# Kernel tuning notes

Measured on AMD Instinct MI355X. Metric: run time of the kernel, lower is better.

## Reference

```python
import jax, jax.numpy as jnp
import numpy as np

B, S, D, H = 4, 1024, 1024, 16
HD = D // H  # head_dim = 64


def setup_inputs() -> dict:
    key = jax.random.key(0)
    ks = jax.random.split(key, 18)
    s = 0.02
    return {
        "x": jax.random.normal(ks[0], (B, S, D), jnp.float32),
        "trust_scores": jax.random.uniform(ks[1], (B, S), jnp.float32),
        "mask": jax.random.randint(ks[2], (B, S), 0, 2).astype(jnp.int32),
        # Linear weights stored as (in, out); torch does x @ W.T + b, equivalent here.
        "Wq": jax.random.normal(ks[3], (D, D), jnp.float32) * s,
        "bq": jnp.zeros((D,), jnp.float32),
        "Wk": jax.random.normal(ks[4], (D, D), jnp.float32) * s,
        "bk": jnp.zeros((D,), jnp.float32),
        "Wv": jax.random.normal(ks[5], (D, D), jnp.float32) * s,
        "bv": jnp.zeros((D,), jnp.float32),
        "Wtp": jax.random.normal(ks[6], (1, HD), jnp.float32) * s,
        "btp": jnp.zeros((HD,), jnp.float32),
        "Wg": jax.random.normal(ks[7], (D + 1, D), jnp.float32) * s,
        "bg": jnp.zeros((D,), jnp.float32),
        "Wo": jax.random.normal(ks[8], (D, D), jnp.float32) * s,
        "bo": jnp.zeros((D,), jnp.float32),
    }


def reference(x, trust_scores, mask, Wq, bq, Wk, bk, Wv, bv, Wtp, btp, Wg, bg, Wo, bo):
    b, s, d = x.shape
    hd = Wtp.shape[1]
    h = d // hd
    # QKV projections -> [b, h, s, hd]
    q = (x @ Wq + bq).reshape(b, s, h, hd).transpose(0, 2, 1, 3)
    k = (x @ Wk + bk).reshape(b, s, h, hd).transpose(0, 2, 1, 3)
    v = (x @ Wv + bv).reshape(b, s, h, hd).transpose(0, 2, 1, 3)
    scores = jnp.einsum("bhqd,bhkd->bhqk", q, k) / jnp.sqrt(jnp.float32(hd))
    # Trust affinity bias: project scalar trust -> head_dim, outer-product + sigmoid.
    trust_proj = trust_scores[:, :, None] @ Wtp + btp  # [b, s, hd]
    trust_aff = jax.nn.sigmoid(jnp.einsum("bqd,bkd->bqk", trust_proj, trust_proj))
    scores = scores + 0.1 * trust_aff[:, None, :, :]  # broadcast over heads
    # Mask applies along the QUERY axis (mask.unsqueeze(1).unsqueeze(-1) in torch).
    scores = jnp.where(mask[:, None, :, None] == 0, jnp.float32(-1e9), scores)
    attn = jax.nn.softmax(scores, axis=-1)  # [b, h, s, s]
    attended = jnp.einsum("bhqk,bhkd->bhqd", attn, v)
    attended = attended.transpose(0, 2, 1, 3).reshape(b, s, d)
    # Trust gate: sigmoid(Linear([attended, trust])) elementwise gate.
    gate_in = jnp.concatenate([attended, trust_scores[:, :, None]], axis=-1)
    gate = jax.nn.sigmoid(gate_in @ Wg + bg)
    attended = attended * gate
    output = attended @ Wo + bo
    return (output, attn)
```

## Files before the change

kernel.cpp:

```cpp
#include <hip/hip_runtime.h>
#include <math.h>

#define BB 4
#define SS 1024
#define DD 1024
#define HH 16
#define HDD 64
#define MTOT (BB*SS)
#define MB (1024*1024)

typedef float  f32x4  __attribute__((ext_vector_type(4)));
typedef __bf16 bf16x8 __attribute__((ext_vector_type(8)));
typedef unsigned short u16;

__device__ __forceinline__ unsigned short f2bf(float f) {
    union { float f; unsigned u; } v; v.f = f;
    unsigned r = v.u + 0x7FFFu + ((v.u >> 16) & 1u);
    return (unsigned short)(r >> 16);
}
__device__ __forceinline__ float bf2f(unsigned short u) {
    union { unsigned u; float f; } v; v.u = ((unsigned)u) << 16;
    return v.f;
}
__device__ __forceinline__ f32x4 mfma16(bf16x8 a, bf16x8 b, f32x4 c) {
    return __builtin_amdgcn_mfma_f32_16x16x32_bf16(a, b, c, 0, 0, 0);
}
__device__ __forceinline__ void gload16(const void* g, void* l) {
    __builtin_amdgcn_global_load_lds(
        (const __attribute__((address_space(1))) void*)g,
        (__attribute__((address_space(3))) void*)l, 16, 0, 0);
}
__device__ __forceinline__ void lds_fence() {
    asm volatile("s_waitcnt lgkmcnt(0)" ::: "memory");
    __builtin_amdgcn_sched_barrier(0);
}

__global__ void split_kernel(const float* __restrict__ in, u16* __restrict__ hi,
                             u16* __restrict__ lo, int n4)
{
    for (int i = blockIdx.x*blockDim.x + threadIdx.x; i < n4; i += gridDim.x*blockDim.x) {
        f32x4 v = ((const f32x4*)in)[i];
        ushort4 h4;
        h4.x = f2bf(v[0]); h4.y = f2bf(v[1]); h4.z = f2bf(v[2]); h4.w = f2bf(v[3]);
        ((ushort4*)hi)[i] = h4;
        if (lo) {
            ushort4 l4v;
            l4v.x = f2bf(v[0] - bf2f(h4.x)); l4v.y = f2bf(v[1] - bf2f(h4.y));
            l4v.z = f2bf(v[2] - bf2f(h4.z)); l4v.w = f2bf(v[3] - bf2f(h4.w));
            ((ushort4*)lo)[i] = l4v;
        }
    }
}

__global__ __launch_bounds__(256)
void tsplit5_kernel(const float* W0, u16* h0,
                    const float* W1, u16* h1,
                    const float* W2, u16* h2,
                    const float* W3, u16* h3,
                    const float* W4, u16* h4, u16* l4T)
{
    const float* W; u16* hT; u16* lT = nullptr;
    switch (blockIdx.z) {
        case 0: W = W0; hT = h0; break;
        case 1: W = W1; hT = h1; break;
        case 2: W = W2; hT = h2; break;
        case 3: W = W3; hT = h3; break;
        default: W = W4; hT = h4; lT = l4T; break;
    }
    __shared__ float tile[64][65];
    const int t  = threadIdx.x;
    const int k0 = blockIdx.y * 64, n0 = blockIdx.x * 64;
    const int r  = t >> 4, c4 = (t & 15) * 4;
    #pragma unroll
    for (int rr = 0; rr < 4; ++rr) {
        const int k = r + rr*16;
        f32x4 v = *(const f32x4*)&W[(size_t)(k0 + k)*1024 + n0 + c4];
        tile[k][c4+0] = v[0]; tile[k][c4+1] = v[1]; tile[k][c4+2] = v[2]; tile[k][c4+3] = v[3];
    }
    __syncthreads();
    #pragma unroll
    for (int rr = 0; rr < 4; ++rr) {
        const int nl = r + rr*16;
        ushort4 hh, ll;
        {
            float v;
            v = tile[c4+0][nl]; hh.x = f2bf(v); ll.x = f2bf(v - bf2f(hh.x));
            v = tile[c4+1][nl]; hh.y = f2bf(v); ll.y = f2bf(v - bf2f(hh.y));
            v = tile[c4+2][nl]; hh.z = f2bf(v); ll.z = f2bf(v - bf2f(hh.z));
            v = tile[c4+3][nl]; hh.w = f2bf(v); ll.w = f2bf(v - bf2f(hh.w));
        }
        *(ushort4*)&hT[(size_t)(n0 + nl)*1024 + k0 + c4] = hh;
        if (lT) *(ushort4*)&lT[(size_t)(n0 + nl)*1024 + k0 + c4] = ll;
    }
}

__global__ void tconst_kernel(const float* __restrict__ Wtp, const float* __restrict__ btp,
                              float* __restrict__ out3)
{
    const int l = threadIdx.x;
    const float w = Wtp[l], b = btp[l];
    float a = w*w, m = w*b, c = b*b;
    #pragma unroll
    for (int s = 32; s; s >>= 1) {
        a += __shfl_down(a, s);
        m += __shfl_down(m, s);
        c += __shfl_down(c, s);
    }
    if (l == 0) { out3[0] = a; out3[1] = m; out3[2] = c; }
}

__global__ __launch_bounds__(256)
void tbias_kernel(const float* __restrict__ trust, const float* __restrict__ tconst,
                  u16* __restrict__ T2)
{
    const int qt = blockIdx.x;
    const int b  = blockIdx.y;
    const int t  = threadIdx.x;
    const int lane = t & 63, grp = t >> 6;
    const int l15 = lane & 15, l4 = lane >> 4;
    const float c1 = tconst[0], c2 = tconst[1], c3 = tconst[2];
    float tq[4];
    #pragma unroll
    for (int r = 0; r < 4; ++r) tq[r] = trust[b*SS + qt*16 + l4*4 + r];
    for (int kt2 = 0; kt2 < 16; ++kt2) {
        const int kt = grp*16 + kt2;
        const float tk = trust[b*SS + kt*16 + l15];
        ushort4 o;
        #pragma unroll
        for (int r = 0; r < 4; ++r) {
            const float ta = c1*tq[r]*tk + c2*(tq[r] + tk) + c3;
            ((u16*)&o)[r] = f2bf(0.1f/(1.f + __expf(-ta)));
        }
        *(ushort4*)&T2[((((size_t)b*64 + qt)*64 + kt)*64 + lane)*4] = o;
    }
}

template<int MODE, int PASSES>
__global__ __launch_bounds__(256)
void mgemm(const u16* __restrict__ Ah, const u16* __restrict__ Al,
           const u16* __restrict__ Bh, const u16* __restrict__ Bl,
           const float* __restrict__ bias,
           float* __restrict__ outF, u16* __restrict__ outH, u16* __restrict__ outL,
           int M, int N,
           const float* __restrict__ trust, const float* __restrict__ wlast,
           const u16* __restrict__ attH, const u16* __restrict__ attL)
{
    constexpr int NT   = (PASSES == 3) ? 4 : (PASSES == 2) ? 3 : 2;
    constexpr int BIDX = (PASSES == 1) ? 1 : 2;
    __shared__ u16 lds[2][NT][128*64];

    const int t    = threadIdx.x;
    const int lane = t & 63, wave = t >> 6;
    const int l15  = lane & 15, l4 = lane >> 4;
    const int wr   = wave >> 1, wc = wave & 1;
    const int w64  = wave << 6;
    const int m0   = blockIdx.y * 128, n0 = blockIdx.x * 128;

    const u16* srcs[NT];
    srcs[0] = Ah + (size_t)m0*1024;
    if (PASSES >= 2) srcs[1] = Al + (size_t)m0*1024;
    if (MODE == 6) {
        srcs[BIDX] = (n0 < 1024) ? Bh + (size_t)n0*1024
                                 : Bl + (size_t)(n0 - 1024)*1024;
    } else {
        srcs[BIDX] = Bh + (size_t)n0*1024;
    }
    if (PASSES == 3) srcs[3] = Bl + (size_t)n0*1024;

    f32x4 acc[4][4];
    #pragma unroll
    for (int i = 0; i < 4; ++i)
        #pragma unroll
        for (int j = 0; j < 4; ++j) acc[i][j] = (f32x4){0.f,0.f,0.f,0.f};

#define STAGE(BUF, KOFF) do {                                                  \
    _Pragma("unroll")                                                          \
    for (int tl_ = 0; tl_ < NT; ++tl_) {                                       \
        _Pragma("unroll")                                                      \
        for (int it_ = 0; it_ < 4; ++it_) {                                    \
            const int idx_ = it_*256 + t;                                      \
            const int row_ = idx_ >> 3;                                        \
            const int c_   = (idx_ & 7) ^ (row_ & 7);                          \
            gload16(srcs[tl_] + (KOFF) + (size_t)row_*1024 + c_*8,             \
                    &lds[BUF][tl_][(it_*256 + w64)*8]);                        \
        }                                                                      \
    }                                                                          \
} while(0)

#define COMPUTE(BUF) do {                                                      \
    _Pragma("unroll")                                                          \
    for (int kk_ = 0; kk_ < 2; ++kk_) {                                        \
        const int cb_ = (kk_<<2) + l4;                                         \
        bf16x8 ah_[4], al_[4];                                                 \
        _Pragma("unroll")                                                      \
        for (int i_ = 0; i_ < 4; ++i_) {                                       \
            const int row_ = (wr<<6) + (i_<<4) + l15;                          \
            const int off_ = (row_<<6) + ((cb_ ^ (row_&7)) << 3);              \
            ah_[i_] = *(const bf16x8*)&lds[BUF][0][off_];                      \
            if (PASSES >= 2) al_[i_] = *(const bf16x8*)&lds[BUF][1][off_];     \
        }                                                                      \
        _Pragma("unroll")                                                      \
        for (int j_ = 0; j_ < 4; ++j_) {                                       \
            const int row_ = (wc<<6) + (j_<<4) + l15;                          \
            const int off_ = (row_<<6) + ((cb_ ^ (row_&7)) << 3);              \
            bf16x8 bh_ = *(const bf16x8*)&lds[BUF][BIDX][off_];                \
            bf16x8 bl_;                                                        \
            if (PASSES == 3) bl_ = *(const bf16x8*)&lds[BUF][3][off_];         \
            _Pragma("unroll")                                                  \
            for (int i_ = 0; i_ < 4; ++i_) {                                   \
                acc[i_][j_] = mfma16(ah_[i_], bh_, acc[i_][j_]);               \
                if (PASSES == 3) acc[i_][j_] = mfma16(ah_[i_], bl_, acc[i_][j_]); \
                if (PASSES >= 2) acc[i_][j_] = mfma16(al_[i_], bh_, acc[i_][j_]); \
            }                                                                  \
        }                                                                      \
    }                                                                          \
} while(0)

    STAGE(0, 0);
    __syncthreads();
    int cur = 0;
    for (int s = 0; s < 15; ++s) {
        if (cur == 0) STAGE(1, (s+1)*64);
        else          STAGE(0, (s+1)*64);
        COMPUTE(cur);
        __syncthreads();
        cur ^= 1;
    }
    COMPUTE(cur);
#undef STAGE
#undef COMPUTE

    #pragma unroll
    for (int i = 0; i < 4; ++i)
        #pragma unroll
        for (int j = 0; j < 4; ++j)
            #pragma unroll
            for (int r = 0; r < 4; ++r) {
                const int m = m0 + (wr<<6) + (i<<4) + (l4<<2) + r;
                const int n = n0 + (wc<<6) + (j<<4) + l15;
                const float v = acc[i][j][r];
                if (MODE == 0) {
                    outF[(size_t)m*N + n] = v + bias[n];
                } else if (MODE == 2) {
                    outH[(size_t)m*N + n] = f2bf(v + bias[n]);
                } else if (MODE == 4) {
                    const size_t blk = (((size_t)((m >> 10)*16 + (n >> 6)))*64
                                        + ((m >> 4) & 63))*1024;
                    outH[blk + ((n & 63) >> 3)*128 + (m & 15)*8 + (n & 7)]
                        = f2bf(v + bias[n]);
                } else if (MODE == 5) {
                    const size_t blk = ((((size_t)((n >> 10)*16 + (m >> 6)))*32
                                        + ((n & 1023) >> 5))*4 + ((m & 63) >> 4))*512;
                    outH[blk + ((n & 31) >> 3)*128 + (m & 15)*8 + (n & 7)]
                        = f2bf(v + bias[m]);
                } else if (MODE == 6) {
                    if (n0 < 1024) {
                        outH[(size_t)m*1024 + n] = f2bf(v + bias[n]);
                    } else {
                        const int nk = n - 1024;
                        const size_t blk = (((size_t)((m >> 10)*16 + (nk >> 6)))*64
                                            + ((m >> 4) & 63))*1024;
                        outL[blk + ((nk & 63) >> 3)*128 + (m & 15)*8 + (nk & 7)]
                            = f2bf(v + wlast[nk]);
                    }
                } else {
                    const float pre = v + bias[n] + trust[m]*wlast[n];
                    const float g = 1.f/(1.f + __expf(-pre));
                    const float att = bf2f(attH[(size_t)m*N + n]) + bf2f(attL[(size_t)m*N + n]);
                    const float gated = att*g;
                    const unsigned short hb = f2bf(gated);
                    outH[(size_t)m*N + n] = hb;
                    outL[(size_t)m*N + n] = f2bf(gated - bf2f(hb));
                }
            }
}

__global__ __launch_bounds__(512, 4)
void attn_kernel(const u16* __restrict__ Qb, const u16* __restrict__ Kf,
                 const u16* __restrict__ Vf, const u16* __restrict__ T,
                 const int* __restrict__ mask,
                 float* __restrict__ attnOut, u16* __restrict__ attH, u16* __restrict__ attL)
{
    __shared__ float Pw[8][16*68 + 16];
    __shared__ float redA[8][16];
    __shared__ float redB[8][16];

    const int t    = threadIdx.x;
    const int lane = t & 63, wave = t >> 6;
    const int l15  = lane & 15, l4 = lane >> 4;

    const int bid  = blockIdx.x;
    const int xcd  = bid & 7;
    const int idx0 = bid >> 3;
    const int p3   = idx0 & 7;
    const int q6   = idx0 >> 3;
    const int q0   = q6 * 16;
    const int b    = xcd >> 1;
    const int h    = ((xcd & 1) << 3) + p3;

    float* myP = Pw[wave];

    int mrow[4];
    #pragma unroll
    for (int r = 0; r < 4; ++r) mrow[r] = mask[b*SS + q0 + l4*4 + r];

    const u16* Qp = Qb + ((size_t)(b*SS + q0 + l15))*DD + h*HDD + l4*8;
    bf16x8 qf0 = *(const bf16x8*)Qp;
    bf16x8 qf1 = *(const bf16x8*)(Qp + 32);

    f32x4 sacc[8];
    #pragma unroll
    for (int tt = 0; tt < 8; ++tt) sacc[tt] = (f32x4){0.f,0.f,0.f,0.f};

    const u16* Kbase = Kf + (((size_t)(b*16 + h))*64 + wave*8)*1024 + l4*128 + l15*8;
    #pragma unroll
    for (int tt = 0; tt < 8; ++tt) {
        bf16x8 kf0 = *(const bf16x8*)(Kbase + tt*1024);
        bf16x8 kf1 = *(const bf16x8*)(Kbase + tt*1024 + 512);
        sacc[tt] = mfma16(qf0, kf0, sacc[tt]);
        sacc[tt] = mfma16(qf1, kf1, sacc[tt]);
    }

    const u16* Tb = T + ((((size_t)b*64 + q6)*64 + wave*8)*64 + lane)*4;
    float mx[4] = {-3e38f, -3e38f, -3e38f, -3e38f};
    #pragma unroll
    for (int tt = 0; tt < 8; ++tt) {
        ushort4 t4 = *(const ushort4*)(Tb + (size_t)tt*256);
        #pragma unroll
        for (int r = 0; r < 4; ++r) {
            const float bias = bf2f(((const u16*)&t4)[r]);
            float s = sacc[tt][r]*0.125f + bias;
            s = mrow[r] ? s : -1e9f;
            sacc[tt][r] = s;
            mx[r] = fmaxf(mx[r], s);
        }
    }
    #pragma unroll
    for (int r = 0; r < 4; ++r)
        #pragma unroll
        for (int xm = 1; xm < 16; xm <<= 1) mx[r] = fmaxf(mx[r], __shfl_xor(mx[r], xm));
    if (l15 == 0) {
        #pragma unroll
        for (int r = 0; r < 4; ++r) redA[wave][l4*4 + r] = mx[r];
    }
    __syncthreads();

    float mxa[4];
    #pragma unroll
    for (int r = 0; r < 4; ++r) {
        const int row = l4*4 + r;
        float m = redA[0][row];
        #pragma unroll
        for (int w = 1; w < 8; ++w) m = fmaxf(m, redA[w][row]);
        mxa[r] = m;
    }

    float sum[4] = {0.f, 0.f, 0.f, 0.f};
    #pragma unroll
    for (int tt = 0; tt < 8; ++tt)
        #pragma unroll
        for (int r = 0; r < 4; ++r) {
            const float p = __expf(sacc[tt][r] - mxa[r]);
            sacc[tt][r] = p;
            sum[r] += p;
        }
    #pragma unroll
    for (int r = 0; r < 4; ++r)
        #pragma unroll
        for (int xm = 1; xm < 16; xm <<= 1) sum[r] += __shfl_xor(sum[r], xm);
    if (l15 == 0) {
        #pragma unroll
        for (int r = 0; r < 4; ++r) redB[wave][l4*4 + r] = sum[r];
    }
    __syncthreads();

    float inv4[4];
    #pragma unroll
    for (int r = 0; r < 4; ++r) {
        const int row = l4*4 + r;
        float s8 = 0.f;
        #pragma unroll
        for (int w = 0; w < 8; ++w) s8 += redB[w][row];
        inv4[r] = 1.f / s8;
    }
    float wiv4[4];
    #pragma unroll
    for (int it = 0; it < 4; ++it) {
        const int row = it*4 + l4;
        float s8 = 0.f;
        #pragma unroll
        for (int w = 0; w < 8; ++w) s8 += redB[w][row];
        wiv4[it] = 1.f / s8;
    }

    float* gBase = attnOut + (((size_t)(b*HH + h))*SS + q0)*SS + wave*128;
    f32x4 pv[4];
    #pragma unroll
    for (int nt = 0; nt < 4; ++nt) pv[nt] = (f32x4){0.f,0.f,0.f,0.f};

    #pragma unroll
    for (int half = 0; half < 2; ++half) {
        #pragma unroll
        for (int t2 = 0; t2 < 4; ++t2)
            #pragma unroll
            for (int r = 0; r < 4; ++r)
                myP[(l4*4 + r)*68 + t2*16 + l15] = sacc[half*4 + t2][r];
        lds_fence();

        #pragma unroll
        for (int it = 0; it < 4; ++it) {
            const int row = it*4 + l4;
            f32x4 v = *(f32x4*)&myP[row*68 + l15*4];
            v *= wiv4[it];
            *(f32x4*)&gBase[(size_t)row*SS + half*64 + l15*4] = v;
        }

        #pragma unroll
        for (int kg = 0; kg < 2; ++kg) {
            const int c0 = kg*32 + l4*8;
            f32x4 a0 = *(f32x4*)&myP[l15*68 + c0];
            f32x4 a1 = *(f32x4*)&myP[l15*68 + c0 + 4];
            bf16x8 af;
            af[0] = (__bf16)a0[0]; af[1] = (__bf16)a0[1]; af[2] = (__bf16)a0[2]; af[3] = (__bf16)a0[3];
            af[4] = (__bf16)a1[0]; af[5] = (__bf16)a1[1]; af[6] = (__bf16)a1[2]; af[7] = (__bf16)a1[3];
            const int kc = wave*4 + half*2 + kg;
            const u16* Vp = Vf + (((size_t)(b*16 + h))*32 + kc)*2048 + l4*128 + l15*8;
            #pragma unroll
            for (int nt = 0; nt < 4; ++nt) {
                bf16x8 bf = *(const bf16x8*)(Vp + nt*512);
                pv[nt] = mfma16(af, bf, pv[nt]);
            }
        }
        lds_fence();
    }

    #pragma unroll
    for (int nt = 0; nt < 4; ++nt)
        #pragma unroll
        for (int r = 0; r < 4; ++r)
            myP[(l4*4 + r)*64 + nt*16 + l15] = pv[nt][r] * inv4[r];
    __syncthreads();

    {
        const int q = t >> 5, d0 = (t & 31)*2;
        float sx = 0.f, sy = 0.f;
        #pragma unroll
        for (int w = 0; w < 8; ++w) {
            float2 v = *(float2*)&Pw[w][q*64 + d0];
            sx += v.x; sy += v.y;
        }
        const size_t off = ((size_t)(b*SS + q0 + q))*DD + h*HDD + d0;
        const unsigned short h0 = f2bf(sx), h1 = f2bf(sy);
        ushort2 hh = {h0, h1};
        ushort2 ll = {f2bf(sx - bf2f(h0)), f2bf(sy - bf2f(h1))};
        *(ushort2*)&attH[off] = hh;
        *(ushort2*)&attL[off] = ll;
    }
}

extern "C" void kernel_launch(void* const* d_in, const int* in_sizes, int n_in,
                              void* d_out, int out_size, void* d_ws, size_t ws_size,
                              hipStream_t stream) {
    const float* x     = (const float*)d_in[0];
    const float* trust = (const float*)d_in[1];
    const int*   mask  = (const int*)  d_in[2];
    const float* Wq    = (const float*)d_in[3];
    const float* bq    = (const float*)d_in[4];
    const float* Wk    = (const float*)d_in[5];
    const float* bk    = (const float*)d_in[6];
    const float* Wv    = (const float*)d_in[7];
    const float* bv    = (const float*)d_in[8];
    const float* Wtp   = (const float*)d_in[9];
    const float* btp   = (const float*)d_in[10];
    const float* Wg    = (const float*)d_in[11];
    const float* bg    = (const float*)d_in[12];
    const float* Wo    = (const float*)d_in[13];
    const float* bo    = (const float*)d_in[14];

    float* out     = (float*)d_out;
    float* attnOut = out + (size_t)MTOT * DD;

    char* ws = (char*)d_ws;
    u16* xh   = (u16*)(ws + (size_t)0*MB);
    u16* attL = (u16*)(ws + (size_t)8*MB);
    u16* WqTh = (u16*)(ws + (size_t)16*MB);
    u16* WkTh = (u16*)(ws + (size_t)18*MB);
    u16* WvTh = (u16*)(ws + (size_t)20*MB);
    u16* WgTh = (u16*)(ws + (size_t)22*MB);
    u16* WoTh = (u16*)(ws + (size_t)24*MB);
    u16* WoTl = (u16*)(ws + (size_t)26*MB);
    u16* Qbf  = (u16*)(ws + (size_t)28*MB);
    u16* Kfb  = (u16*)(ws + (size_t)36*MB);
    u16* Vfb  = (u16*)(ws + (size_t)44*MB);
    u16* Tb   = (u16*)(ws + (size_t)52*MB);
    float* tconst = (float*)(ws + (size_t)60*MB);
    u16* attH = xh;
    u16* Gh   = Qbf;
    u16* Gl   = Kfb;

    const dim3 blk(256);

    tconst_kernel<<<1, 64, 0, stream>>>(Wtp, btp, tconst);
    tbias_kernel<<<dim3(64, BB), blk, 0, stream>>>(trust, tconst, Tb);
    split_kernel<<<2048, blk, 0, stream>>>(x, xh, nullptr, MTOT*DD/4);
    tsplit5_kernel<<<dim3(16, 16, 5), blk, 0, stream>>>(
        Wq, WqTh, Wk, WkTh, Wv, WvTh, Wg, WgTh, Wo, WoTh, WoTl);

    mgemm<6,1><<<dim3(2048/128, MTOT/128), blk, 0, stream>>>(
        xh, nullptr, WqTh, WkTh, bq, nullptr, Qbf, Kfb, MTOT, 2048,
        nullptr, bk, nullptr, nullptr);
    mgemm<5,1><<<dim3(MTOT/128, DD/128), blk, 0, stream>>>(
        WvTh, nullptr, xh, nullptr, bv, nullptr, Vfb, nullptr, DD, MTOT,
        nullptr, nullptr, nullptr, nullptr);

    attn_kernel<<<dim3(4096), dim3(512), 0, stream>>>(
        Qbf, Kfb, Vfb, Tb, mask, attnOut, attH, attL);

    mgemm<1,1><<<dim3(DD/128, MTOT/128), blk, 0, stream>>>(
        attH, nullptr, WgTh, nullptr, bg, nullptr, Gh, Gl, MTOT, DD,
        trust, Wg + (size_t)DD*DD, attH, attL);
    mgemm<0,3><<<dim3(DD/128, MTOT/128), blk, 0, stream>>>(
        Gh, Gl, WoTh, WoTl, bo, out, nullptr, nullptr, MTOT, DD,
        nullptr, nullptr, nullptr, nullptr);
}
```

Baseline: 241.7 us.

## Drop hi/lo bf16 split for output GEMM and fuse V projection into QKV GEMM

Removes the two-term bf16 error-compensation path: attention output, gated activations and Wo are now kept only as single bf16 values, so the final GEMM runs one MFMA pass instead of three and the lo buffers are no longer written or read. The V projection is folded into the Q/K GEMM launch (N=3072), with a third output region written in V's blocked layout, which removes one kernel launch and one reread of x. The cost is lower accuracy in the output projection, and an output-mode routing that reuses parameter slots for different pointers (trust holds bk, wlast holds bv, attH holds the Wv weights).

```diff
diff --git a/kernel.cpp b/kernel.cpp
--- a/kernel.cpp
+++ b/kernel.cpp
@@ -35,20 +35,13 @@
     __builtin_amdgcn_sched_barrier(0);
 }
 
-__global__ void split_kernel(const float* __restrict__ in, u16* __restrict__ hi,
-                             u16* __restrict__ lo, int n4)
+__global__ void split_kernel(const float* __restrict__ in, u16* __restrict__ hi, int n4)
 {
     for (int i = blockIdx.x*blockDim.x + threadIdx.x; i < n4; i += gridDim.x*blockDim.x) {
         f32x4 v = ((const f32x4*)in)[i];
         ushort4 h4;
         h4.x = f2bf(v[0]); h4.y = f2bf(v[1]); h4.z = f2bf(v[2]); h4.w = f2bf(v[3]);
         ((ushort4*)hi)[i] = h4;
-        if (lo) {
-            ushort4 l4v;
-            l4v.x = f2bf(v[0] - bf2f(h4.x)); l4v.y = f2bf(v[1] - bf2f(h4.y));
-            l4v.z = f2bf(v[2] - bf2f(h4.z)); l4v.w = f2bf(v[3] - bf2f(h4.w));
-            ((ushort4*)lo)[i] = l4v;
-        }
     }
 }
 
@@ -57,15 +50,15 @@
                     const float* W1, u16* h1,
                     const float* W2, u16* h2,
                     const float* W3, u16* h3,
-                    const float* W4, u16* h4, u16* l4T)
-{
-    const float* W; u16* hT; u16* lT = nullptr;
+                    const float* W4, u16* h4)
+{
+    const float* W; u16* hT;
     switch (blockIdx.z) {
         case 0: W = W0; hT = h0; break;
         case 1: W = W1; hT = h1; break;
         case 2: W = W2; hT = h2; break;
         case 3: W = W3; hT = h3; break;
-        default: W = W4; hT = h4; lT = l4T; break;
+        default: W = W4; hT = h4; break;
     }
     __shared__ float tile[64][65];
     const int t  = threadIdx.x;
@@ -81,16 +74,10 @@
     #pragma unroll
     for (int rr = 0; rr < 4; ++rr) {
         const int nl = r + rr*16;
-        ushort4 hh, ll;
-        {
-            float v;
-            v = tile[c4+0][nl]; hh.x = f2bf(v); ll.x = f2bf(v - bf2f(hh.x));
-            v = tile[c4+1][nl]; hh.y = f2bf(v); ll.y = f2bf(v - bf2f(hh.y));
-            v = tile[c4+2][nl]; hh.z = f2bf(v); ll.z = f2bf(v - bf2f(hh.z));
-            v = tile[c4+3][nl]; hh.w = f2bf(v); ll.w = f2bf(v - bf2f(hh.w));
-        }
+        ushort4 hh;
+        hh.x = f2bf(tile[c4+0][nl]); hh.y = f2bf(tile[c4+1][nl]);
+        hh.z = f2bf(tile[c4+2][nl]); hh.w = f2bf(tile[c4+3][nl]);
         *(ushort4*)&hT[(size_t)(n0 + nl)*1024 + k0 + c4] = hh;
-        if (lT) *(ushort4*)&lT[(size_t)(n0 + nl)*1024 + k0 + c4] = ll;
     }
 }
 
@@ -143,7 +130,7 @@
            float* __restrict__ outF, u16* __restrict__ outH, u16* __restrict__ outL,
            int M, int N,
            const float* __restrict__ trust, const float* __restrict__ wlast,
-           const u16* __restrict__ attH, const u16* __restrict__ attL)
+           const u16* __restrict__ attH)
 {
     constexpr int NT   = (PASSES == 3) ? 4 : (PASSES == 2) ? 3 : 2;
     constexpr int BIDX = (PASSES == 1) ? 1 : 2;
@@ -159,9 +146,10 @@
     const u16* srcs[NT];
     srcs[0] = Ah + (size_t)m0*1024;
     if (PASSES >= 2) srcs[1] = Al + (size_t)m0*1024;
-    if (MODE == 6) {
+    if (MODE == 7) {
         srcs[BIDX] = (n0 < 1024) ? Bh + (size_t)n0*1024
-                                 : Bl + (size_t)(n0 - 1024)*1024;
+                   : (n0 < 2048) ? Bl + (size_t)(n0 - 1024)*1024
+                                 : attH + (size_t)(n0 - 2048)*1024;
     } else {
         srcs[BIDX] = Bh + (size_t)n0*1024;
     }
@@ -241,36 +229,28 @@
                 const float v = acc[i][j][r];
                 if (MODE == 0) {
                     outF[(size_t)m*N + n] = v + bias[n];
-                } else if (MODE == 2) {
-                    outH[(size_t)m*N + n] = f2bf(v + bias[n]);
-                } else if (MODE == 4) {
-                    const size_t blk = (((size_t)((m >> 10)*16 + (n >> 6)))*64
-                                        + ((m >> 4) & 63))*1024;
-                    outH[blk + ((n & 63) >> 3)*128 + (m & 15)*8 + (n & 7)]
-                        = f2bf(v + bias[n]);
-                } else if (MODE == 5) {
-                    const size_t blk = ((((size_t)((n >> 10)*16 + (m >> 6)))*32
-                                        + ((n & 1023) >> 5))*4 + ((m & 63) >> 4))*512;
-                    outH[blk + ((n & 31) >> 3)*128 + (m & 15)*8 + (n & 7)]
-                        = f2bf(v + bias[m]);
-                } else if (MODE == 6) {
-                    if (n0 < 1024) {
+                } else if (MODE == 7) {
+                    if (n < 1024) {
                         outH[(size_t)m*1024 + n] = f2bf(v + bias[n]);
-                    } else {
+                    } else if (n < 2048) {
                         const int nk = n - 1024;
                         const size_t blk = (((size_t)((m >> 10)*16 + (nk >> 6)))*64
                                             + ((m >> 4) & 63))*1024;
                         outL[blk + ((nk & 63) >> 3)*128 + (m & 15)*8 + (nk & 7)]
-                            = f2bf(v + wlast[nk]);
+                            = f2bf(v + trust[nk]);
+                    } else {
+                        const int nv = n - 2048;
+                        u16* outV = (u16*)outF;
+                        const size_t blk = ((((size_t)((m >> 10)*16 + (nv >> 6)))*32
+                                            + ((m & 1023) >> 5))*4 + ((nv & 63) >> 4))*512;
+                        outV[blk + ((m & 31) >> 3)*128 + (nv & 15)*8 + (m & 7)]
+                            = f2bf(v + wlast[nv]);
                     }
                 } else {
                     const float pre = v + bias[n] + trust[m]*wlast[n];
                     const float g = 1.f/(1.f + __expf(-pre));
-                    const float att = bf2f(attH[(size_t)m*N + n]) + bf2f(attL[(size_t)m*N + n]);
-                    const float gated = att*g;
-                    const unsigned short hb = f2bf(gated);
-                    outH[(size_t)m*N + n] = hb;
-                    outL[(size_t)m*N + n] = f2bf(gated - bf2f(hb));
+                    const float att = bf2f(attH[(size_t)m*N + n]);
+                    outH[(size_t)m*N + n] = f2bf(att*g);
                 }
             }
 }
@@ -279,7 +259,7 @@
 void attn_kernel(const u16* __restrict__ Qb, const u16* __restrict__ Kf,
                  const u16* __restrict__ Vf, const u16* __restrict__ T,
                  const int* __restrict__ mask,
-                 float* __restrict__ attnOut, u16* __restrict__ attH, u16* __restrict__ attL)
+                 float* __restrict__ attnOut, u16* __restrict__ attH)
 {
     __shared__ float Pw[8][16*68 + 16];
     __shared__ float redA[8][16];
@@ -450,11 +430,8 @@
             sx += v.x; sy += v.y;
         }
         const size_t off = ((size_t)(b*SS + q0 + q))*DD + h*HDD + d0;
-        const unsigned short h0 = f2bf(sx), h1 = f2bf(sy);
-        ushort2 hh = {h0, h1};
-        ushort2 ll = {f2bf(sx - bf2f(h0)), f2bf(sy - bf2f(h1))};
+        ushort2 hh = {f2bf(sx), f2bf(sy)};
         *(ushort2*)&attH[off] = hh;
-        *(ushort2*)&attL[off] = ll;
     }
 }
 
@@ -482,13 +459,11 @@
 
     char* ws = (char*)d_ws;
     u16* xh   = (u16*)(ws + (size_t)0*MB);
-    u16* attL = (u16*)(ws + (size_t)8*MB);
     u16* WqTh = (u16*)(ws + (size_t)16*MB);
     u16* WkTh = (u16*)(ws + (size_t)18*MB);
     u16* WvTh = (u16*)(ws + (size_t)20*MB);
     u16* WgTh = (u16*)(ws + (size_t)22*MB);
     u16* WoTh = (u16*)(ws + (size_t)24*MB);
-    u16* WoTl = (u16*)(ws + (size_t)26*MB);
     u16* Qbf  = (u16*)(ws + (size_t)28*MB);
     u16* Kfb  = (u16*)(ws + (size_t)36*MB);
     u16* Vfb  = (u16*)(ws + (size_t)44*MB);
@@ -496,30 +471,26 @@
     float* tconst = (float*)(ws + (size_t)60*MB);
     u16* attH = xh;
     u16* Gh   = Qbf;
-    u16* Gl   = Kfb;
 
     const dim3 blk(256);
 
     tconst_kernel<<<1, 64, 0, stream>>>(Wtp, btp, tconst);
     tbias_kernel<<<dim3(64, BB), blk, 0, stream>>>(trust, tconst, Tb);
-    split_kernel<<<2048, blk, 0, stream>>>(x, xh, nullptr, MTOT*DD/4);
+    split_kernel<<<2048, blk, 0, stream>>>(x, xh, MTOT*DD/4);
     tsplit5_kernel<<<dim3(16, 16, 5), blk, 0, stream>>>(
-        Wq, WqTh, Wk, WkTh, Wv, WvTh, Wg, WgTh, Wo, WoTh, WoTl);
-
-    mgemm<6,1><<<dim3(2048/128, MTOT/128), blk, 0, stream>>>(
-        xh, nullptr, WqTh, WkTh, bq, nullptr, Qbf, Kfb, MTOT, 2048,
-        nullptr, bk, nullptr, nullptr);
-    mgemm<5,1><<<dim3(MTOT/128, DD/128), blk, 0, stream>>>(
-        WvTh, nullptr, xh, nullptr, bv, nullptr, Vfb, nullptr, DD, MTOT,
-        nullptr, nullptr, nullptr, nullptr);
+        Wq, WqTh, Wk, WkTh, Wv, WvTh, Wg, WgTh, Wo, WoTh);
+
+    mgemm<7,1><<<dim3(3072/128, MTOT/128), blk, 0, stream>>>(
+        xh, nullptr, WqTh, WkTh, bq, (float*)Vfb, Qbf, Kfb, MTOT, 3072,
+        bk, bv, WvTh);
 
     attn_kernel<<<dim3(4096), dim3(512), 0, stream>>>(
-        Qbf, Kfb, Vfb, Tb, mask, attnOut, attH, attL);
+        Qbf, Kfb, Vfb, Tb, mask, attnOut, attH);
 
     mgemm<1,1><<<dim3(DD/128, MTOT/128), blk, 0, stream>>>(
-        attH, nullptr, WgTh, nullptr, bg, nullptr, Gh, Gl, MTOT, DD,
-        trust, Wg + (size_t)DD*DD, attH, attL);
-    mgemm<0,3><<<dim3(DD/128, MTOT/128), blk, 0, stream>>>(
-        Gh, Gl, WoTh, WoTl, bo, out, nullptr, nullptr, MTOT, DD,
-        nullptr, nullptr, nullptr, nullptr);
-}
+        attH, nullptr, WgTh, nullptr, bg, nullptr, Gh, nullptr, MTOT, DD,
+        trust, Wg + (size_t)DD*DD, attH);
+    mgemm<0,1><<<dim3(DD/128, MTOT/128), blk, 0, stream>>>(
+        Gh, nullptr, WoTh, nullptr, bo, out, nullptr, nullptr, MTOT, DD,
+        nullptr, nullptr, nullptr);
+}
```

Measured after the change: 233.4 us. 3.4% less time.
